# Kernel optimization log

Hardware: AMD Instinct MI355X
Metric: run time of the kernel (lower is better)

## Reference

```python
import jax, jax.numpy as jnp
import numpy as np

N, E, H = 100000, 640000, 64
DIN_N, DIN_E, L, OUT = 32, 16, 2, 1
BN_EPS = 1e-5


def setup_inputs() -> dict:
    key = jax.random.key(0)
    ks = iter(jax.random.split(key, 40))
    def p(shape, s=0.05):
        return jax.random.normal(next(ks), shape, dtype=jnp.float32) * s
    return {
        "x": jax.random.normal(next(ks), (N, DIN_N), dtype=jnp.float32),
        "edge_attr": jax.random.normal(next(ks), (E, DIN_E), dtype=jnp.float32),
        "src": jax.random.randint(next(ks), (E,), 0, N),
        "dst": jax.random.randint(next(ks), (E,), 0, N),
        "node_emb_w": p((DIN_N, H)), "node_emb_b": p((H,)),
        "edge_emb_w": p((DIN_E, H)), "edge_emb_b": p((H,)),
        "lin_edge_w": p((L, H, H)), "lin_edge_b": p((L, H)),
        "conv_w1": p((L, H, H)), "conv_b1": p((L, H)),
        "conv_w2": p((L, H, H)), "conv_b2": p((L, H)),
        "emlp_w1": p((L, 3 * H, H)), "emlp_b1": p((L, H)),
        "emlp_w2": p((L, H, H)), "emlp_b2": p((L, H)),
        "bn_gamma": jnp.ones((L, H), jnp.float32),
        "bn_beta": jnp.zeros((L, H), jnp.float32),
        "mlp_w1": p((3 * H, 50)), "mlp_b1": p((50,)),
        "mlp_w2": p((50, 25)), "mlp_b2": p((25,)),
        "mlp_w3": p((25, OUT)), "mlp_b3": p((OUT,)),
    }


def _batchnorm(h, gamma, beta):
    # training-mode BatchNorm1d over the node axis (biased variance)
    mu = jnp.mean(h, axis=0)
    var = jnp.mean(jnp.square(h - mu), axis=0)
    return gamma * (h - mu) * jax.lax.rsqrt(var + BN_EPS) + beta


def _forward(x, edge_attr, src, dst,
             node_emb_w, node_emb_b, edge_emb_w, edge_emb_b,
             lin_edge_w, lin_edge_b, conv_w1, conv_b1, conv_w2, conv_b2,
             emlp_w1, emlp_b1, emlp_w2, emlp_b2, bn_gamma, bn_beta,
             mlp_w1, mlp_b1, mlp_w2, mlp_b2, mlp_w3, mlp_b3):
    x = x @ node_emb_w + node_emb_b                       # [N, H]
    e = edge_attr @ edge_emb_w + edge_emb_b               # [E, H]
    for i in range(L):
        # GINEConv (eps=0): msg = ReLU(x_src + Lin(edge_attr)); sum at dst
        msg = jax.nn.relu(x[src] + e @ lin_edge_w[i] + lin_edge_b[i])
        agg = jax.ops.segment_sum(msg, dst, num_segments=N)
        h = x + agg
        h = jax.nn.relu(h @ conv_w1[i] + conv_b1[i]) @ conv_w2[i] + conv_b2[i]
        x = (x + jax.nn.relu(_batchnorm(h, bn_gamma[i], bn_beta[i]))) / 2
        cat = jnp.concatenate([x[src], x[dst], e], axis=-1)  # [E, 3H]
        upd = jax.nn.relu(cat @ emlp_w1[i] + emlp_b1[i]) @ emlp_w2[i] + emlp_b2[i]
        e = e + upd / 2
    # edge readout: relu(cat(x_src, x_dst)) ++ edge_attr -> MLP (dropout off/eval)
    er = jnp.concatenate(
        [jax.nn.relu(jnp.concatenate([x[src], x[dst]], axis=-1)), e], axis=-1)
    hmid = jax.nn.relu(er @ mlp_w1 + mlp_b1)
    hmid = jax.nn.relu(hmid @ mlp_w2 + mlp_b2)
    logit = hmid @ mlp_w3 + mlp_b3
    return x, logit


def reference(x, edge_attr, src, dst,
              node_emb_w, node_emb_b, edge_emb_w, edge_emb_b,
              lin_edge_w, lin_edge_b, conv_w1, conv_b1, conv_w2, conv_b2,
              emlp_w1, emlp_b1, emlp_w2, emlp_b2, bn_gamma, bn_beta,
              mlp_w1, mlp_b1, mlp_w2, mlp_b2, mlp_w3, mlp_b3):
    return _forward(x, edge_attr, src, dst,
                    node_emb_w, node_emb_b, edge_emb_w, edge_emb_b,
                    lin_edge_w, lin_edge_b, conv_w1, conv_b1, conv_w2, conv_b2,
                    emlp_w1, emlp_b1, emlp_w2, emlp_b2, bn_gamma, bn_beta,
                    mlp_w1, mlp_b1, mlp_w2, mlp_b2, mlp_w3, mlp_b3)
```

## Files before the change

kernel.cpp:

```cpp
#include <hip/hip_runtime.h>

#define NN 100000
#define NE 640000
#define NB_SCAN 98

typedef __attribute__((ext_vector_type(8))) short short8;
typedef __attribute__((ext_vector_type(4))) float f32x4;
typedef __attribute__((ext_vector_type(4))) ushort ushort4v;

__device__ __forceinline__ float bf2f(ushort u) {
    unsigned v = ((unsigned)u) << 16;
    return __builtin_bit_cast(float, v);
}
__device__ __forceinline__ ushort f2bf(float f) {
    unsigned u = __builtin_bit_cast(unsigned, f);
    u += 0x7fffu + ((u >> 16) & 1u);
    return (ushort)(u >> 16);
}
__device__ __forceinline__ short8 brelu(short8 v) {
    #pragma unroll
    for (int i = 0; i < 8; ++i) v[i] = (v[i] < (short)0) ? (short)0 : v[i];
    return v;
}

__global__ void k_hist(const int* __restrict__ dst, int* __restrict__ hist)
{
    int i = blockIdx.x * 256 + threadIdx.x;
    atomicAdd(&hist[dst[i]], 1);
}

__global__ __launch_bounds__(256) void k_scan_part(const int* __restrict__ hist,
                                                   int* __restrict__ rp,
                                                   int* __restrict__ parts)
{
    __shared__ int s[256];
    int b = blockIdx.x, t = threadIdx.x;
    int base = b * 1024 + t * 4;
    int v[4]; int sum = 0;
    #pragma unroll
    for (int i = 0; i < 4; ++i) { int idx = base + i; v[i] = (idx < NN) ? hist[idx] : 0; sum += v[i]; }
    s[t] = sum; __syncthreads();
    for (int off = 1; off < 256; off <<= 1) {
        int x = (t >= off) ? s[t - off] : 0;
        __syncthreads(); s[t] += x; __syncthreads();
    }
    int excl = s[t] - sum;
    if (t == 255) parts[b] = s[255];
    int run = excl;
    #pragma unroll
    for (int i = 0; i < 4; ++i) { int idx = base + i; if (idx < NN) rp[idx] = run; run += v[i]; }
}

__global__ void k_scan_tops(int* __restrict__ parts, int* __restrict__ rp)
{
    __shared__ int s[128];
    int t = threadIdx.x;
    int v = (t < NB_SCAN) ? parts[t] : 0;
    s[t] = v; __syncthreads();
    for (int off = 1; off < 128; off <<= 1) {
        int x = (t >= off) ? s[t - off] : 0;
        __syncthreads(); s[t] += x; __syncthreads();
    }
    parts[t] = s[t] - v;
    if (t == 0) rp[NN] = NE;
}

__global__ __launch_bounds__(256) void k_scan_add(int* __restrict__ rp,
                                                  const int* __restrict__ parts,
                                                  int* __restrict__ cursor)
{
    int i = blockIdx.x * 256 + threadIdx.x;
    if (i >= NN) return;
    int v = rp[i] + parts[i >> 10];
    rp[i] = v; cursor[i] = v;
}

__global__ void k_scatter(const int* __restrict__ dst,
                          int* __restrict__ cursor, int* __restrict__ eidx)
{
    int i = blockIdx.x * 256 + threadIdx.x;
    int d = dst[i];
    int p = atomicAdd(&cursor[d], 1);
    eidx[p] = i;
}

__global__ void k_w_subtile(const float* __restrict__ w, ushort* __restrict__ out,
                            int K, int Nin)
{
    int t = blockIdx.x * 256 + threadIdx.x;
    if (t >= K * 64) return;
    int k = t >> 6, c = t & 63;
    float v = (c < Nin) ? w[k * Nin + c] : 0.f;
    out[((k >> 3) * 64 + c) * 8 + (k & 7)] = f2bf(v);
}

__global__ void k_w_padk(const float* __restrict__ w, ushort* __restrict__ out,
                         int Kreal, int Kpad)
{
    int t = blockIdx.x * 256 + threadIdx.x;
    if (t >= Kpad * 64) return;
    int k = t >> 6, c = t & 63;
    float v = (k < Kreal) ? w[k * 64 + c] : 0.f;
    out[((k >> 3) * 64 + c) * 8 + (k & 7)] = f2bf(v);
}

__global__ void k_w_msg(const float* __restrict__ lw, ushort* __restrict__ out)
{
    int t = blockIdx.x * 256 + threadIdx.x;
    if (t >= 128 * 64) return;
    int k = t >> 6, c = t & 63;
    float v = (k < 64) ? (k == c ? 1.f : 0.f) : lw[(k - 64) * 64 + c];
    out[((k >> 3) * 64 + c) * 8 + (k & 7)] = f2bf(v);
}

__global__ __launch_bounds__(256) void k_node_emb_mfma(
    const float* __restrict__ xin, const ushort* __restrict__ ws,
    const float* __restrict__ b, float* __restrict__ xout,
    ushort* __restrict__ xb)
{
    __shared__ ushort wl[32 * 64];
    __shared__ float fbuf[4][16 * 64];
    __shared__ ushort bbuf[4][16 * 64];
    int tid = threadIdx.x;
    *(short8*)&wl[tid * 8] = *(const short8*)&ws[tid * 8];
    __syncthreads();

    int wid = tid >> 6, lane = tid & 63, c = lane & 15, kg = lane >> 4;
    int t = blockIdx.x * 4 + wid;
    if (t >= NN / 16) return;
    int n0 = t * 16;

    const float* xr = xin + (size_t)(n0 + c) * 32 + kg * 8;
    f32x4 u0 = *(const f32x4*)xr, u1 = *(const f32x4*)(xr + 4);
    short8 a;
    #pragma unroll
    for (int j = 0; j < 4; ++j) { a[j] = (short)f2bf(u0[j]); a[4 + j] = (short)f2bf(u1[j]); }

    f32x4 acc[4];
    #pragma unroll
    for (int nt = 0; nt < 4; ++nt) {
        float bv = b[nt * 16 + c];
        acc[nt] = f32x4{bv, bv, bv, bv};
        short8 bf = *(const short8*)&wl[(kg * 64 + nt * 16 + c) * 8];
        acc[nt] = __builtin_amdgcn_mfma_f32_16x16x32_bf16(a, bf, acc[nt], 0, 0, 0);
    }
    #pragma unroll
    for (int nt = 0; nt < 4; ++nt)
        #pragma unroll
        for (int i = 0; i < 4; ++i) {
            int rr = kg * 4 + i, cc = nt * 16 + c;
            float v = acc[nt][i];
            fbuf[wid][rr * 64 + cc] = v;
            bbuf[wid][rr * 64 + cc] = f2bf(v);
        }
    #pragma unroll
    for (int r = 0; r < 4; ++r) {
        int q = r * 64 + lane;
        *(f32x4*)&xout[(size_t)(n0 + (q >> 4)) * 64 + (q & 15) * 4] =
            *(f32x4*)&fbuf[wid][q * 4];
    }
    #pragma unroll
    for (int r = 0; r < 2; ++r) {
        int q = r * 64 + lane;
        *(short8*)&xb[(size_t)(n0 + (q >> 3)) * 64 + (q & 7) * 8] =
            *(short8*)&bbuf[wid][q * 8];
    }
}

__global__ __launch_bounds__(256) void k_edge_emb_fused(
    const float* __restrict__ ein, const ushort* __restrict__ ws,
    const float* __restrict__ b, ushort* __restrict__ eb,
    const ushort* __restrict__ xb, const int* __restrict__ src,
    const ushort* __restrict__ wm, const float* __restrict__ lb,
    ushort* __restrict__ msgbuf)
{
    __shared__ ushort wl[32 * 64];
    __shared__ ushort wml[128 * 64];
    __shared__ ushort bbuf[4][16 * 72];
    int tid = threadIdx.x;
    *(short8*)&wl[tid * 8] = *(const short8*)&ws[tid * 8];
    #pragma unroll
    for (int i = 0; i < 4; ++i)
        *(short8*)&wml[(i * 256 + tid) * 8] = *(const short8*)&wm[(i * 256 + tid) * 8];
    __syncthreads();

    int wid = tid >> 6, lane = tid & 63, c = lane & 15, kg = lane >> 4;
    int e0 = (blockIdx.x * 4 + wid) * 16;
    ushort* bb = bbuf[wid];

    const ushort* xs = xb + (size_t)src[e0 + c] * 64;
    short8 a0 = *(const short8*)(xs + kg * 8);
    short8 a1 = *(const short8*)(xs + 32 + kg * 8);

    short8 a = (short8)0;
    if (kg < 2) {
        const float* er = ein + (size_t)(e0 + c) * 16 + kg * 8;
        f32x4 u0 = *(const f32x4*)er, u1 = *(const f32x4*)(er + 4);
        #pragma unroll
        for (int j = 0; j < 4; ++j) { a[j] = (short)f2bf(u0[j]); a[4 + j] = (short)f2bf(u1[j]); }
    }
    f32x4 acc[4];
    #pragma unroll
    for (int nt = 0; nt < 4; ++nt) {
        float bv = b[nt * 16 + c];
        acc[nt] = f32x4{bv, bv, bv, bv};
        short8 bf = *(const short8*)&wl[(kg * 64 + nt * 16 + c) * 8];
        acc[nt] = __builtin_amdgcn_mfma_f32_16x16x32_bf16(a, bf, acc[nt], 0, 0, 0);
    }
    #pragma unroll
    for (int nt = 0; nt < 4; ++nt)
        #pragma unroll
        for (int i = 0; i < 4; ++i)
            bb[(kg * 4 + i) * 72 + nt * 16 + c] = f2bf(acc[nt][i]);
    #pragma unroll
    for (int r = 0; r < 2; ++r) {
        int q = r * 64 + lane;
        *(short8*)&eb[(size_t)(e0 + (q >> 3)) * 64 + (q & 7) * 8] =
            *(short8*)&bb[(q >> 3) * 72 + (q & 7) * 8];
    }
    short8 en0 = *(const short8*)&bb[c * 72 + kg * 8];
    short8 en1 = *(const short8*)&bb[c * 72 + 32 + kg * 8];

    f32x4 acc3[4];
    #pragma unroll
    for (int nt = 0; nt < 4; ++nt) {
        float bv = lb[nt * 16 + c];
        acc3[nt] = f32x4{bv, bv, bv, bv};
    }
    short8 af[4] = {a0, a1, en0, en1};
    #pragma unroll
    for (int ks = 0; ks < 4; ++ks) {
        #pragma unroll
        for (int nt = 0; nt < 4; ++nt) {
            short8 bf = *(const short8*)&wml[((ks * 4 + kg) * 64 + nt * 16 + c) * 8];
            acc3[nt] = __builtin_amdgcn_mfma_f32_16x16x32_bf16(af[ks], bf, acc3[nt], 0, 0, 0);
        }
    }
    #pragma unroll
    for (int nt = 0; nt < 4; ++nt)
        #pragma unroll
        for (int i = 0; i < 4; ++i)
            bb[(kg * 4 + i) * 72 + nt * 16 + c] = f2bf(fmaxf(acc3[nt][i], 0.f));
    #pragma unroll
    for (int r = 0; r < 2; ++r) {
        int q = r * 64 + lane;
        *(short8*)&msgbuf[(size_t)(e0 + (q >> 3)) * 64 + (q & 7) * 8] =
            *(short8*)&bb[(q >> 3) * 72 + (q & 7) * 8];
    }
}

__global__ __launch_bounds__(256) void k_conv_csr(
    const float* __restrict__ x, const ushort* __restrict__ msgbuf,
    const int* __restrict__ rp, const int* __restrict__ eidx,
    float* __restrict__ hout,
    const ushort* __restrict__ w1s, const float* __restrict__ b1,
    const ushort* __restrict__ w2s, const float* __restrict__ b2,
    float* __restrict__ stats)
{
    __shared__ ushort w1l[64 * 64];
    __shared__ ushort w2l[64 * 64];
    __shared__ ushort h1l[4][1024];
    __shared__ float red[2][4][64];
    int tid = threadIdx.x;
    #pragma unroll
    for (int i = 0; i < 2; ++i) {
        *(short8*)&w1l[(i * 256 + tid) * 8] = *(const short8*)&w1s[(i * 256 + tid) * 8];
        *(short8*)&w2l[(i * 256 + tid) * 8] = *(const short8*)&w2s[(i * 256 + tid) * 8];
    }
    __syncthreads();

    int wid = tid >> 6, lane = tid & 63;
    int c = lane & 15, kg = lane >> 4;

    short8 w2f[2][4];
    #pragma unroll
    for (int ks = 0; ks < 2; ++ks)
        #pragma unroll
        for (int nt = 0; nt < 4; ++nt)
            w2f[ks][nt] = *(const short8*)&w2l[((ks * 4 + kg) * 64 + nt * 16 + c) * 8];

    float b1v[4], b2v[4];
    #pragma unroll
    for (int nt = 0; nt < 4; ++nt) { b1v[nt] = b1[nt * 16 + c]; b2v[nt] = b2[nt * 16 + c]; }

    float s1[4] = {0.f, 0.f, 0.f, 0.f}, s2[4] = {0.f, 0.f, 0.f, 0.f};
    ushort* hl = h1l[wid];

    int t = blockIdx.x * 4 + wid;
    if (t < NN / 16) {
        int n0 = t * 16;
        int n = n0 + c;
        int jb = rp[n], je = rp[n + 1];
        float sm0[8] = {0,0,0,0,0,0,0,0}, sm1[8] = {0,0,0,0,0,0,0,0};
        if (jb < je) {
            int row = eidx[jb];
            short8 m0 = *(const short8*)&msgbuf[(size_t)row * 64 + kg * 8];
            short8 m1 = *(const short8*)&msgbuf[(size_t)row * 64 + 32 + kg * 8];
            for (int j = jb + 1; j <= je; ++j) {
                short8 p0, p1;
                if (j < je) {
                    int nrow = eidx[j];
                    p0 = *(const short8*)&msgbuf[(size_t)nrow * 64 + kg * 8];
                    p1 = *(const short8*)&msgbuf[(size_t)nrow * 64 + 32 + kg * 8];
                }
                #pragma unroll
                for (int i = 0; i < 8; ++i) {
                    sm0[i] += bf2f((ushort)m0[i]);
                    sm1[i] += bf2f((ushort)m1[i]);
                }
                if (j < je) { m0 = p0; m1 = p1; }
            }
        }
        const float* xr = x + (size_t)n * 64;
        f32x4 u0 = *(const f32x4*)(xr + kg * 8);
        f32x4 u1 = *(const f32x4*)(xr + kg * 8 + 4);
        f32x4 v0 = *(const f32x4*)(xr + 32 + kg * 8);
        f32x4 v1 = *(const f32x4*)(xr + 32 + kg * 8 + 4);
        short8 a[2];
        #pragma unroll
        for (int j = 0; j < 4; ++j) {
            a[0][j]     = (short)f2bf(u0[j] + sm0[j]);
            a[0][4 + j] = (short)f2bf(u1[j] + sm0[4 + j]);
            a[1][j]     = (short)f2bf(v0[j] + sm1[j]);
            a[1][4 + j] = (short)f2bf(v1[j] + sm1[4 + j]);
        }
        f32x4 acc[4];
        #pragma unroll
        for (int nt = 0; nt < 4; ++nt) acc[nt] = f32x4{b1v[nt], b1v[nt], b1v[nt], b1v[nt]};
        #pragma unroll
        for (int ks = 0; ks < 2; ++ks) {
            #pragma unroll
            for (int nt = 0; nt < 4; ++nt) {
                short8 bf = *(const short8*)&w1l[((ks * 4 + kg) * 64 + nt * 16 + c) * 8];
                acc[nt] = __builtin_amdgcn_mfma_f32_16x16x32_bf16(a[ks], bf, acc[nt], 0, 0, 0);
            }
        }
        #pragma unroll
        for (int nt = 0; nt < 4; ++nt) {
            #pragma unroll
            for (int i = 0; i < 4; ++i) {
                int rr = kg * 4 + i, cc = nt * 16 + c;
                hl[((cc >> 3) * 16 + rr) * 8 + (cc & 7)] = f2bf(fmaxf(acc[nt][i], 0.f));
            }
        }
        f32x4 acc2[4];
        #pragma unroll
        for (int nt = 0; nt < 4; ++nt) acc2[nt] = f32x4{b2v[nt], b2v[nt], b2v[nt], b2v[nt]};
        #pragma unroll
        for (int ks = 0; ks < 2; ++ks) {
            short8 ha = *(const short8*)&hl[((ks * 4 + kg) * 16 + c) * 8];
            #pragma unroll
            for (int nt = 0; nt < 4; ++nt)
                acc2[nt] = __builtin_amdgcn_mfma_f32_16x16x32_bf16(ha, w2f[ks][nt], acc2[nt], 0, 0, 0);
        }
        #pragma unroll
        for (int nt = 0; nt < 4; ++nt) {
            #pragma unroll
            for (int i = 0; i < 4; ++i) {
                int rr = kg * 4 + i, cc = nt * 16 + c;
                float h2 = acc2[nt][i];
                hout[(size_t)(n0 + rr) * 64 + cc] = h2;
                s1[nt] += h2;
                s2[nt] += h2 * h2;
            }
        }
    }
    #pragma unroll
    for (int nt = 0; nt < 4; ++nt) {
        float v1 = s1[nt], v2 = s2[nt];
        v1 += __shfl_xor(v1, 16); v1 += __shfl_xor(v1, 32);
        v2 += __shfl_xor(v2, 16); v2 += __shfl_xor(v2, 32);
        s1[nt] = v1; s2[nt] = v2;
    }
    if (lane < 16) {
        #pragma unroll
        for (int nt = 0; nt < 4; ++nt) {
            red[0][wid][nt * 16 + c] = s1[nt];
            red[1][wid][nt * 16 + c] = s2[nt];
        }
    }
    __syncthreads();
    if (wid == 0) {
        float a = red[0][0][lane] + red[0][1][lane] + red[0][2][lane] + red[0][3][lane];
        float b = red[1][0][lane] + red[1][1][lane] + red[1][2][lane] + red[1][3][lane];
        unsafeAtomicAdd(&stats[lane], a);
        unsafeAtomicAdd(&stats[64 + lane], b);
    }
}

__global__ void k_bnfin(float* __restrict__ stats,
                        const float* __restrict__ gamma,
                        const float* __restrict__ beta)
{
    int j = threadIdx.x;
    float mu = stats[j] * (1.f / NN);
    float var = stats[64 + j] * (1.f / NN) - mu * mu;
    float a = gamma[j] * rsqrtf(var + 1e-5f);
    stats[128 + j] = a;
    stats[192 + j] = beta[j] - mu * a;
}

__global__ __launch_bounds__(256) void k_xupd4(float* __restrict__ x,
                                               const float* __restrict__ h,
                                               const float* __restrict__ stats,
                                               ushort* __restrict__ xb)
{
    int idx = blockIdx.x * 256 + threadIdx.x;
    int j4 = (idx & 15) * 4;
    f32x4 hv = *(const f32x4*)&h[(size_t)idx * 4];
    f32x4 xv = *(const f32x4*)&x[(size_t)idx * 4];
    f32x4 av = *(const f32x4*)&stats[128 + j4];
    f32x4 cv = *(const f32x4*)&stats[192 + j4];
    f32x4 xo;
    ushort4v bo;
    #pragma unroll
    for (int i = 0; i < 4; ++i) {
        float r = fmaxf(fmaf(hv[i], av[i], cv[i]), 0.f);
        float xn = (xv[i] + r) * 0.5f;
        xo[i] = xn;
        bo[i] = f2bf(xn);
    }
    *(f32x4*)&x[(size_t)idx * 4] = xo;
    *(ushort4v*)&xb[(size_t)idx * 4] = bo;
}

template<int NEXT>
__global__ __launch_bounds__(256) void k_emlp_fused(
    const ushort* __restrict__ xb, ushort* __restrict__ eb,
    const int* __restrict__ src, const int* __restrict__ dst,
    const ushort* __restrict__ w1s, const float* __restrict__ b1,
    const ushort* __restrict__ w2s, const float* __restrict__ b2,
    const ushort* __restrict__ wm, const float* __restrict__ lbn,
    ushort* __restrict__ msgbuf)
{
    __shared__ ushort w1l[192 * 64];
    __shared__ ushort wml[NEXT ? 128 * 64 : 8];
    __shared__ ushort hb[4][1152];
    int tid = threadIdx.x;
    #pragma unroll
    for (int i = 0; i < 6; ++i)
        *(short8*)&w1l[(i * 256 + tid) * 8] = *(const short8*)&w1s[(i * 256 + tid) * 8];
    if (NEXT) {
        #pragma unroll
        for (int i = 0; i < 4; ++i)
            *(short8*)&wml[(i * 256 + tid) * 8] = *(const short8*)&wm[(i * 256 + tid) * 8];
    }
    __syncthreads();

    int wid = tid >> 6, lane = tid & 63;
    int c = lane & 15, kg = lane >> 4;

    short8 w2f[2][4];
    #pragma unroll
    for (int ks = 0; ks < 2; ++ks)
        #pragma unroll
        for (int nt = 0; nt < 4; ++nt)
            w2f[ks][nt] = *(const short8*)&w2s[((ks * 4 + kg) * 64 + nt * 16 + c) * 8];

    float b1v[4], b2v[4], lbv[4];
    #pragma unroll
    for (int nt = 0; nt < 4; ++nt) {
        b1v[nt] = b1[nt * 16 + c];
        b2v[nt] = b2[nt * 16 + c];
        lbv[nt] = NEXT ? lbn[nt * 16 + c] : 0.f;
    }
    ushort* hl = hb[wid];

    int ebase = blockIdx.x * 256 + wid * 64;

    short8 a[6];
    {
        int myedge = ebase + c;
        int s = src[myedge], d = dst[myedge];
        const ushort* xs = xb + (size_t)s * 64;
        const ushort* xd = xb + (size_t)d * 64;
        const ushort* ee = eb + (size_t)myedge * 64;
        a[0] = *(const short8*)(xs + kg * 8);
        a[1] = *(const short8*)(xs + 32 + kg * 8);
        a[2] = *(const short8*)(xd + kg * 8);
        a[3] = *(const short8*)(xd + 32 + kg * 8);
        a[4] = *(const short8*)(ee + kg * 8);
        a[5] = *(const short8*)(ee + 32 + kg * 8);
    }

    #pragma unroll 1
    for (int t4 = 0; t4 < 4; ++t4) {
        int e0 = ebase + t4 * 16;
        int myedge = e0 + c;

        short8 an[6];
        if (t4 < 3) {
            int sn = src[myedge + 16];
            int dn = dst[myedge + 16];
            const ushort* xsn = xb + (size_t)sn * 64;
            const ushort* xdn = xb + (size_t)dn * 64;
            const ushort* een = eb + (size_t)(myedge + 16) * 64;
            an[0] = *(const short8*)(xsn + kg * 8);
            an[1] = *(const short8*)(xsn + 32 + kg * 8);
            an[2] = *(const short8*)(xdn + kg * 8);
            an[3] = *(const short8*)(xdn + 32 + kg * 8);
            an[4] = *(const short8*)(een + kg * 8);
            an[5] = *(const short8*)(een + 32 + kg * 8);
        }

        f32x4 acc[4];
        #pragma unroll
        for (int nt = 0; nt < 4; ++nt) acc[nt] = f32x4{b1v[nt], b1v[nt], b1v[nt], b1v[nt]};
        #pragma unroll
        for (int ks = 0; ks < 6; ++ks) {
            #pragma unroll
            for (int nt = 0; nt < 4; ++nt) {
                short8 bf = *(const short8*)&w1l[((ks * 4 + kg) * 64 + nt * 16 + c) * 8];
                acc[nt] = __builtin_amdgcn_mfma_f32_16x16x32_bf16(a[ks], bf, acc[nt], 0, 0, 0);
            }
        }
        #pragma unroll
        for (int nt = 0; nt < 4; ++nt) {
            #pragma unroll
            for (int i = 0; i < 4; ++i) {
                int rr = kg * 4 + i, cc = nt * 16 + c;
                hl[((cc >> 3) * 16 + rr) * 8 + (cc & 7)] = f2bf(fmaxf(acc[nt][i], 0.f));
            }
        }
        f32x4 acc2[4];
        #pragma unroll
        for (int nt = 0; nt < 4; ++nt) acc2[nt] = f32x4{b2v[nt], b2v[nt], b2v[nt], b2v[nt]};
        #pragma unroll
        for (int ks = 0; ks < 2; ++ks) {
            short8 ha = *(const short8*)&hl[((ks * 4 + kg) * 16 + c) * 8];
            #pragma unroll
            for (int nt = 0; nt < 4; ++nt)
                acc2[nt] = __builtin_amdgcn_mfma_f32_16x16x32_bf16(ha, w2f[ks][nt], acc2[nt], 0, 0, 0);
        }
        #pragma unroll
        for (int nt = 0; nt < 4; ++nt)
            #pragma unroll
            for (int i = 0; i < 4; ++i)
                hl[(kg * 4 + i) * 72 + nt * 16 + c] = f2bf(acc2[nt][i]);
        short8 u0 = *(const short8*)&hl[c * 72 + kg * 8];
        short8 u1 = *(const short8*)&hl[c * 72 + 32 + kg * 8];
        short8 en0, en1;
        #pragma unroll
        for (int j = 0; j < 8; ++j) {
            en0[j] = (short)f2bf(bf2f((ushort)a[4][j]) + 0.5f * bf2f((ushort)u0[j]));
            en1[j] = (short)f2bf(bf2f((ushort)a[5][j]) + 0.5f * bf2f((ushort)u1[j]));
        }
        *(short8*)&eb[(size_t)myedge * 64 + kg * 8]      = en0;
        *(short8*)&eb[(size_t)myedge * 64 + 32 + kg * 8] = en1;

        if (NEXT) {
            f32x4 acc3[4];
            #pragma unroll
            for (int nt = 0; nt < 4; ++nt) acc3[nt] = f32x4{lbv[nt], lbv[nt], lbv[nt], lbv[nt]};
            short8 af[4] = {a[0], a[1], en0, en1};
            #pragma unroll
            for (int ks = 0; ks < 4; ++ks) {
                #pragma unroll
                for (int nt = 0; nt < 4; ++nt) {
                    short8 bf = *(const short8*)&wml[((ks * 4 + kg) * 64 + nt * 16 + c) * 8];
                    acc3[nt] = __builtin_amdgcn_mfma_f32_16x16x32_bf16(af[ks], bf, acc3[nt], 0, 0, 0);
                }
            }
            #pragma unroll
            for (int nt = 0; nt < 4; ++nt)
                #pragma unroll
                for (int i = 0; i < 4; ++i)
                    hl[(kg * 4 + i) * 72 + nt * 16 + c] = f2bf(fmaxf(acc3[nt][i], 0.f));
            #pragma unroll
            for (int r = 0; r < 2; ++r) {
                int q = r * 64 + lane;
                *(short8*)&msgbuf[(size_t)(e0 + (q >> 3)) * 64 + (q & 7) * 8] =
                    *(short8*)&hl[(q >> 3) * 72 + (q & 7) * 8];
            }
        }

        if (t4 < 3) {
            #pragma unroll
            for (int i = 0; i < 6; ++i) a[i] = an[i];
        }
    }
}

__global__ __launch_bounds__(256) void k_readout_mfma(
    const ushort* __restrict__ xb, const ushort* __restrict__ eb,
    const int* __restrict__ src, const int* __restrict__ dst,
    const ushort* __restrict__ w1s, const float* __restrict__ b1,
    const float* __restrict__ w2, const float* __restrict__ b2,
    const float* __restrict__ w3, const float* __restrict__ b3,
    float* __restrict__ logit)
{
    __shared__ ushort w1l[192 * 64];
    __shared__ ushort hw[4][64 * 50];
    int tid = threadIdx.x;
    #pragma unroll
    for (int i = 0; i < 6; ++i)
        *(short8*)&w1l[(i * 256 + tid) * 8] = *(const short8*)&w1s[(i * 256 + tid) * 8];
    __syncthreads();

    int wid = tid >> 6, lane = tid & 63;
    int c = lane & 15, kg = lane >> 4;
    float b1v[4];
    #pragma unroll
    for (int nt = 0; nt < 4; ++nt) b1v[nt] = (nt * 16 + c < 50) ? b1[nt * 16 + c] : 0.f;

    int ebase = blockIdx.x * 256 + wid * 64;

    short8 a[6];
    {
        int myedge = ebase + c;
        int s = src[myedge], d = dst[myedge];
        const ushort* xs = xb + (size_t)s * 64;
        const ushort* xd = xb + (size_t)d * 64;
        const ushort* ee = eb + (size_t)myedge * 64;
        a[0] = *(const short8*)(xs + kg * 8);
        a[1] = *(const short8*)(xs + 32 + kg * 8);
        a[2] = *(const short8*)(xd + kg * 8);
        a[3] = *(const short8*)(xd + 32 + kg * 8);
        a[4] = *(const short8*)(ee + kg * 8);
        a[5] = *(const short8*)(ee + 32 + kg * 8);
    }

    #pragma unroll 1
    for (int t4 = 0; t4 < 4; ++t4) {
        int e0 = ebase + t4 * 16;
        int myedge = e0 + c;

        short8 an[6];
        if (t4 < 3) {
            int sn = src[myedge + 16];
            int dn = dst[myedge + 16];
            const ushort* xsn = xb + (size_t)sn * 64;
            const ushort* xdn = xb + (size_t)dn * 64;
            const ushort* een = eb + (size_t)(myedge + 16) * 64;
            an[0] = *(const short8*)(xsn + kg * 8);
            an[1] = *(const short8*)(xsn + 32 + kg * 8);
            an[2] = *(const short8*)(xdn + kg * 8);
            an[3] = *(const short8*)(xdn + 32 + kg * 8);
            an[4] = *(const short8*)(een + kg * 8);
            an[5] = *(const short8*)(een + 32 + kg * 8);
        }

        short8 af[6];
        af[0] = brelu(a[0]); af[1] = brelu(a[1]);
        af[2] = brelu(a[2]); af[3] = brelu(a[3]);
        af[4] = a[4];        af[5] = a[5];

        f32x4 acc[4];
        #pragma unroll
        for (int nt = 0; nt < 4; ++nt) acc[nt] = f32x4{b1v[nt], b1v[nt], b1v[nt], b1v[nt]};
        #pragma unroll
        for (int ks = 0; ks < 6; ++ks) {
            #pragma unroll
            for (int nt = 0; nt < 4; ++nt) {
                short8 bf = *(const short8*)&w1l[((ks * 4 + kg) * 64 + nt * 16 + c) * 8];
                acc[nt] = __builtin_amdgcn_mfma_f32_16x16x32_bf16(af[ks], bf, acc[nt], 0, 0, 0);
            }
        }
        #pragma unroll
        for (int nt = 0; nt < 4; ++nt) {
            #pragma unroll
            for (int i = 0; i < 4; ++i) {
                int rr = kg * 4 + i, cc = nt * 16 + c;
                if (cc < 50)
                    hw[wid][(t4 * 16 + rr) * 50 + cc] = f2bf(fmaxf(acc[nt][i], 0.f));
            }
        }
        if (t4 < 3) {
            #pragma unroll
            for (int i = 0; i < 6; ++i) a[i] = an[i];
        }
    }
    int edge = blockIdx.x * 256 + wid * 64 + lane;
    const ushort* hrow = &hw[wid][lane * 50];
    float a25[25];
    #pragma unroll
    for (int j = 0; j < 25; ++j) a25[j] = b2[j];
    #pragma unroll 2
    for (int k = 0; k < 50; ++k) {
        float hv = bf2f(hrow[k]);
        #pragma unroll
        for (int j = 0; j < 25; ++j) a25[j] = fmaf(hv, w2[k * 25 + j], a25[j]);
    }
    float lg = b3[0];
    #pragma unroll
    for (int k = 0; k < 25; ++k) lg = fmaf(fmaxf(a25[k], 0.f), w3[k], lg);
    logit[edge] = lg;
}

extern "C" void kernel_launch(void* const* d_in, const int* in_sizes, int n_in,
                              void* d_out, int out_size, void* d_ws, size_t ws_size,
                              hipStream_t stream)
{
    const float* x_in  = (const float*)d_in[0];
    const float* eattr = (const float*)d_in[1];
    const int*   src   = (const int*)d_in[2];
    const int*   dst   = (const int*)d_in[3];
    const float* n_w   = (const float*)d_in[4];
    const float* n_b   = (const float*)d_in[5];
    const float* e_w   = (const float*)d_in[6];
    const float* e_b   = (const float*)d_in[7];
    const float* lw    = (const float*)d_in[8];
    const float* lb    = (const float*)d_in[9];
    const float* cw1   = (const float*)d_in[10];
    const float* cb1   = (const float*)d_in[11];
    const float* cw2   = (const float*)d_in[12];
    const float* cb2   = (const float*)d_in[13];
    const float* ew1   = (const float*)d_in[14];
    const float* eb1   = (const float*)d_in[15];
    const float* ew2   = (const float*)d_in[16];
    const float* eb2   = (const float*)d_in[17];
    const float* gam   = (const float*)d_in[18];
    const float* bet   = (const float*)d_in[19];
    const float* m1w   = (const float*)d_in[20];
    const float* m1b   = (const float*)d_in[21];
    const float* m2w   = (const float*)d_in[22];
    const float* m2b   = (const float*)d_in[23];
    const float* m3w   = (const float*)d_in[24];
    const float* m3b   = (const float*)d_in[25];

    float* xbuf  = (float*)d_out;
    float* logit = xbuf + (size_t)NN * 64;

    ushort* eb     = (ushort*)d_ws;
    float*  tmp    = (float*)(eb + (size_t)NE * 64);
    float*  stats  = tmp + (size_t)NN * 64;
    ushort* w1s    = (ushort*)(stats + 512);
    ushort* w2s    = w1s + 2 * 192 * 64;
    ushort* m1s    = w2s + 2 * 64 * 64;
    ushort* xb     = m1s + 192 * 64;
    ushort* wms    = xb + (size_t)NN * 64;
    ushort* cw1s   = wms + 2 * 128 * 64;
    ushort* cw2s   = cw1s + 2 * 64 * 64;
    ushort* nws    = cw2s + 2 * 64 * 64;
    ushort* ews    = nws + 32 * 64;
    ushort* msgbuf = ews + 32 * 64;
    int*    hist   = (int*)(msgbuf + (size_t)NE * 64);
    int*    rp     = hist + NN;
    int*    cursor = rp + NN + 1;
    int*    parts  = cursor + NN;
    int*    eidx   = parts + 128;

    hipMemsetAsync(hist, 0, NN * sizeof(int), stream);
    hipMemsetAsync(stats, 0, 512 * sizeof(float), stream);
    k_hist<<<NE / 256, 256, 0, stream>>>(dst, hist);
    k_scan_part<<<NB_SCAN, 256, 0, stream>>>(hist, rp, parts);
    k_scan_tops<<<1, 128, 0, stream>>>(parts, rp);
    k_scan_add<<<(NN + 255) / 256, 256, 0, stream>>>(rp, parts, cursor);
    k_scatter<<<NE / 256, 256, 0, stream>>>(dst, cursor, eidx);

    k_w_subtile<<<48, 256, 0, stream>>>(ew1,            w1s,            192, 64);
    k_w_subtile<<<48, 256, 0, stream>>>(ew1 + 192 * 64, w1s + 192 * 64, 192, 64);
    k_w_subtile<<<16, 256, 0, stream>>>(ew2,            w2s,            64, 64);
    k_w_subtile<<<16, 256, 0, stream>>>(ew2 + 64 * 64,  w2s + 64 * 64,  64, 64);
    k_w_subtile<<<48, 256, 0, stream>>>(m1w,            m1s,            192, 50);
    k_w_msg<<<32, 256, 0, stream>>>(lw,           wms);
    k_w_msg<<<32, 256, 0, stream>>>(lw + 64 * 64, wms + 128 * 64);
    k_w_subtile<<<16, 256, 0, stream>>>(cw1,            cw1s,           64, 64);
    k_w_subtile<<<16, 256, 0, stream>>>(cw1 + 64 * 64,  cw1s + 64 * 64, 64, 64);
    k_w_subtile<<<16, 256, 0, stream>>>(cw2,            cw2s,           64, 64);
    k_w_subtile<<<16, 256, 0, stream>>>(cw2 + 64 * 64,  cw2s + 64 * 64, 64, 64);
    k_w_padk<<<8, 256, 0, stream>>>(n_w, nws, 32, 32);
    k_w_padk<<<8, 256, 0, stream>>>(e_w, ews, 16, 32);

    k_node_emb_mfma<<<(NN / 16 + 3) / 4, 256, 0, stream>>>(x_in, nws, n_b, xbuf, xb);
    k_edge_emb_fused<<<NE / 64, 256, 0, stream>>>(eattr, ews, e_b, eb,
                                                  xb, src, wms, lb, msgbuf);

    for (int l = 0; l < 2; ++l) {
        float* st = stats + l * 256;
        k_conv_csr<<<(NN / 16 + 3) / 4, 256, 0, stream>>>(
            xbuf, msgbuf, rp, eidx, tmp, cw1s + l * 64 * 64, cb1 + l * 64,
            cw2s + l * 64 * 64, cb2 + l * 64, st);
        k_bnfin<<<1, 64, 0, stream>>>(st, gam + l * 64, bet + l * 64);
        k_xupd4<<<NN * 16 / 256, 256, 0, stream>>>(xbuf, tmp, st, xb);
        if (l == 0) {
            k_emlp_fused<1><<<NE / 256, 256, 0, stream>>>(
                xb, eb, src, dst, w1s, eb1, w2s, eb2,
                wms + 128 * 64, lb + 64, msgbuf);
        } else {
            k_emlp_fused<0><<<NE / 256, 256, 0, stream>>>(
                xb, eb, src, dst, w1s + 192 * 64, eb1 + 64, w2s + 64 * 64, eb2 + 64,
                wms, lb, msgbuf);
        }
    }

    k_readout_mfma<<<NE / 256, 256, 0, stream>>>(xb, eb, src, dst,
                                                 m1s, m1b, m2w, m2b, m3w, m3b, logit);
}
```

Measured before the change: 537.4 us.

## Process two 16-edge tiles per iteration in edge MLP kernel, move W2 to LDS

The fused edge-MLP kernel now handles two 16-edge tiles (A and B) per loop iteration, interleaving their MFMA chains so independent work can hide MFMA latency. It prefetches the next pair of tiles' gathers after the first GEMM. The second-layer weights move from per-thread register fragments into shared memory to free registers for the doubled accumulators and operands. LDS use grows (double h buffer plus W2), and register pressure rises, which may lower occupancy.

Result: slower. 562.6 us (+4.7%).

```diff
diff --git a/kernel.cpp b/kernel.cpp
--- a/kernel.cpp
+++ b/kernel.cpp
@@ -434,12 +434,16 @@
     ushort* __restrict__ msgbuf)
 {
     __shared__ ushort w1l[192 * 64];
+    __shared__ ushort w2l[64 * 64];
     __shared__ ushort wml[NEXT ? 128 * 64 : 8];
-    __shared__ ushort hb[4][1152];
+    __shared__ ushort hb[4][2304];
     int tid = threadIdx.x;
     #pragma unroll
     for (int i = 0; i < 6; ++i)
         *(short8*)&w1l[(i * 256 + tid) * 8] = *(const short8*)&w1s[(i * 256 + tid) * 8];
+    #pragma unroll
+    for (int i = 0; i < 2; ++i)
+        *(short8*)&w2l[(i * 256 + tid) * 8] = *(const short8*)&w2s[(i * 256 + tid) * 8];
     if (NEXT) {
         #pragma unroll
         for (int i = 0; i < 4; ++i)
@@ -449,13 +453,6 @@
 
     int wid = tid >> 6, lane = tid & 63;
     int c = lane & 15, kg = lane >> 4;
-
-    short8 w2f[2][4];
-    #pragma unroll
-    for (int ks = 0; ks < 2; ++ks)
-        #pragma unroll
-        for (int nt = 0; nt < 4; ++nt)
-            w2f[ks][nt] = *(const short8*)&w2s[((ks * 4 + kg) * 64 + nt * 16 + c) * 8];
 
     float b1v[4], b2v[4], lbv[4];
     #pragma unroll
@@ -464,119 +461,176 @@
         b2v[nt] = b2[nt * 16 + c];
         lbv[nt] = NEXT ? lbn[nt * 16 + c] : 0.f;
     }
-    ushort* hl = hb[wid];
+    ushort* hlA = hb[wid];
+    ushort* hlB = hb[wid] + 1152;
 
     int ebase = blockIdx.x * 256 + wid * 64;
 
-    short8 a[6];
+    short8 aA[6], aB[6];
     {
-        int myedge = ebase + c;
-        int s = src[myedge], d = dst[myedge];
-        const ushort* xs = xb + (size_t)s * 64;
-        const ushort* xd = xb + (size_t)d * 64;
-        const ushort* ee = eb + (size_t)myedge * 64;
-        a[0] = *(const short8*)(xs + kg * 8);
-        a[1] = *(const short8*)(xs + 32 + kg * 8);
-        a[2] = *(const short8*)(xd + kg * 8);
-        a[3] = *(const short8*)(xd + 32 + kg * 8);
-        a[4] = *(const short8*)(ee + kg * 8);
-        a[5] = *(const short8*)(ee + 32 + kg * 8);
+        int mA = ebase + c, mB = ebase + 16 + c;
+        int sA = src[mA], dA = dst[mA];
+        int sB = src[mB], dB = dst[mB];
+        const ushort* xsA = xb + (size_t)sA * 64;
+        const ushort* xdA = xb + (size_t)dA * 64;
+        const ushort* eeA = eb + (size_t)mA * 64;
+        const ushort* xsB = xb + (size_t)sB * 64;
+        const ushort* xdB = xb + (size_t)dB * 64;
+        const ushort* eeB = eb + (size_t)mB * 64;
+        aA[0] = *(const short8*)(xsA + kg * 8);
+        aA[1] = *(const short8*)(xsA + 32 + kg * 8);
+        aA[2] = *(const short8*)(xdA + kg * 8);
+        aA[3] = *(const short8*)(xdA + 32 + kg * 8);
+        aA[4] = *(const short8*)(eeA + kg * 8);
+        aA[5] = *(const short8*)(eeA + 32 + kg * 8);
+        aB[0] = *(const short8*)(xsB + kg * 8);
+        aB[1] = *(const short8*)(xsB + 32 + kg * 8);
+        aB[2] = *(const short8*)(xdB + kg * 8);
+        aB[3] = *(const short8*)(xdB + 32 + kg * 8);
+        aB[4] = *(const short8*)(eeB + kg * 8);
+        aB[5] = *(const short8*)(eeB + 32 + kg * 8);
     }
 
     #pragma unroll 1
-    for (int t4 = 0; t4 < 4; ++t4) {
-        int e0 = ebase + t4 * 16;
-        int myedge = e0 + c;
-
-        short8 an[6];
-        if (t4 < 3) {
-            int sn = src[myedge + 16];
-            int dn = dst[myedge + 16];
-            const ushort* xsn = xb + (size_t)sn * 64;
-            const ushort* xdn = xb + (size_t)dn * 64;
-            const ushort* een = eb + (size_t)(myedge + 16) * 64;
-            an[0] = *(const short8*)(xsn + kg * 8);
-            an[1] = *(const short8*)(xsn + 32 + kg * 8);
-            an[2] = *(const short8*)(xdn + kg * 8);
-            an[3] = *(const short8*)(xdn + 32 + kg * 8);
-            an[4] = *(const short8*)(een + kg * 8);
-            an[5] = *(const short8*)(een + 32 + kg * 8);
-        }
-
-        f32x4 acc[4];
-        #pragma unroll
-        for (int nt = 0; nt < 4; ++nt) acc[nt] = f32x4{b1v[nt], b1v[nt], b1v[nt], b1v[nt]};
+    for (int pr = 0; pr < 2; ++pr) {
+        int e0A = ebase + pr * 32;
+        int e0B = e0A + 16;
+        int mA = e0A + c, mB = e0B + c;
+
+        f32x4 accA[4], accB[4];
+        #pragma unroll
+        for (int nt = 0; nt < 4; ++nt) {
+            accA[nt] = f32x4{b1v[nt], b1v[nt], b1v[nt], b1v[nt]};
+            accB[nt] = f32x4{b1v[nt], b1v[nt], b1v[nt], b1v[nt]};
+        }
         #pragma unroll
         for (int ks = 0; ks < 6; ++ks) {
             #pragma unroll
             for (int nt = 0; nt < 4; ++nt) {
                 short8 bf = *(const short8*)&w1l[((ks * 4 + kg) * 64 + nt * 16 + c) * 8];
-                acc[nt] = __builtin_amdgcn_mfma_f32_16x16x32_bf16(a[ks], bf, acc[nt], 0, 0, 0);
-            }
-        }
+                accA[nt] = __builtin_amdgcn_mfma_f32_16x16x32_bf16(aA[ks], bf, accA[nt], 0, 0, 0);
+                accB[nt] = __builtin_amdgcn_mfma_f32_16x16x32_bf16(aB[ks], bf, accB[nt], 0, 0, 0);
+            }
+        }
+
+        short8 nA[6], nB[6];
+        if (pr == 0) {
+            int pA = mA + 32, pB = mB + 32;
+            int sA = src[pA], dA = dst[pA];
+            int sB = src[pB], dB = dst[pB];
+            const ushort* xsA = xb + (size_t)sA * 64;
+            const ushort* xdA = xb + (size_t)dA * 64;
+            const ushort* eeA = eb + (size_t)pA * 64;
+            const ushort* xsB = xb + (size_t)sB * 64;
+            const ushort* xdB = xb + (size_t)dB * 64;
+            const ushort* eeB = eb + (size_t)pB * 64;
+            nA[0] = *(const short8*)(xsA + kg * 8);
+            nA[1] = *(const short8*)(xsA + 32 + kg * 8);
+            nA[2] = *(const short8*)(xdA + kg * 8);
+            nA[3] = *(const short8*)(xdA + 32 + kg * 8);
+            nA[4] = *(const short8*)(eeA + kg * 8);
+            nA[5] = *(const short8*)(eeA + 32 + kg * 8);
+            nB[0] = *(const short8*)(xsB + kg * 8);
+            nB[1] = *(const short8*)(xsB + 32 + kg * 8);
+            nB[2] = *(const short8*)(xdB + kg * 8);
+            nB[3] = *(const short8*)(xdB + 32 + kg * 8);
+            nB[4] = *(const short8*)(eeB + kg * 8);
+            nB[5] = *(const short8*)(eeB + 32 + kg * 8);
+        }
+
         #pragma unroll
         for (int nt = 0; nt < 4; ++nt) {
             #pragma unroll
             for (int i = 0; i < 4; ++i) {
                 int rr = kg * 4 + i, cc = nt * 16 + c;
-                hl[((cc >> 3) * 16 + rr) * 8 + (cc & 7)] = f2bf(fmaxf(acc[nt][i], 0.f));
-            }
-        }
-        f32x4 acc2[4];
-        #pragma unroll
-        for (int nt = 0; nt < 4; ++nt) acc2[nt] = f32x4{b2v[nt], b2v[nt], b2v[nt], b2v[nt]};
+                int off = ((cc >> 3) * 16 + rr) * 8 + (cc & 7);
+                hlA[off] = f2bf(fmaxf(accA[nt][i], 0.f));
+                hlB[off] = f2bf(fmaxf(accB[nt][i], 0.f));
+            }
+        }
+        f32x4 a2A[4], a2B[4];
+        #pragma unroll
+        for (int nt = 0; nt < 4; ++nt) {
+            a2A[nt] = f32x4{b2v[nt], b2v[nt], b2v[nt], b2v[nt]};
+            a2B[nt] = f32x4{b2v[nt], b2v[nt], b2v[nt], b2v[nt]};
+        }
         #pragma unroll
         for (int ks = 0; ks < 2; ++ks) {
-            short8 ha = *(const short8*)&hl[((ks * 4 + kg) * 16 + c) * 8];
-            #pragma unroll
-            for (int nt = 0; nt < 4; ++nt)
-                acc2[nt] = __builtin_amdgcn_mfma_f32_16x16x32_bf16(ha, w2f[ks][nt], acc2[nt], 0, 0, 0);
-        }
-        #pragma unroll
-        for (int nt = 0; nt < 4; ++nt)
-            #pragma unroll
-            for (int i = 0; i < 4; ++i)
-                hl[(kg * 4 + i) * 72 + nt * 16 + c] = f2bf(acc2[nt][i]);
-        short8 u0 = *(const short8*)&hl[c * 72 + kg * 8];
-        short8 u1 = *(const short8*)&hl[c * 72 + 32 + kg * 8];
-        short8 en0, en1;
+            short8 haA = *(const short8*)&hlA[((ks * 4 + kg) * 16 + c) * 8];
+            short8 haB = *(const short8*)&hlB[((ks * 4 + kg) * 16 + c) * 8];
+            #pragma unroll
+            for (int nt = 0; nt < 4; ++nt) {
+                short8 bw = *(const short8*)&w2l[((ks * 4 + kg) * 64 + nt * 16 + c) * 8];
+                a2A[nt] = __builtin_amdgcn_mfma_f32_16x16x32_bf16(haA, bw, a2A[nt], 0, 0, 0);
+                a2B[nt] = __builtin_amdgcn_mfma_f32_16x16x32_bf16(haB, bw, a2B[nt], 0, 0, 0);
+            }
+        }
+        #pragma unroll
+        for (int nt = 0; nt < 4; ++nt) {
+            #pragma unroll
+            for (int i = 0; i < 4; ++i) {
+                int off = (kg * 4 + i) * 72 + nt * 16 + c;
+                hlA[off] = f2bf(a2A[nt][i]);
+                hlB[off] = f2bf(a2B[nt][i]);
+            }
+        }
+        short8 u0A = *(const short8*)&hlA[c * 72 + kg * 8];
+        short8 u1A = *(const short8*)&hlA[c * 72 + 32 + kg * 8];
+        short8 u0B = *(const short8*)&hlB[c * 72 + kg * 8];
+        short8 u1B = *(const short8*)&hlB[c * 72 + 32 + kg * 8];
+        short8 enA0, enA1, enB0, enB1;
         #pragma unroll
         for (int j = 0; j < 8; ++j) {
-            en0[j] = (short)f2bf(bf2f((ushort)a[4][j]) + 0.5f * bf2f((ushort)u0[j]));
-            en1[j] = (short)f2bf(bf2f((ushort)a[5][j]) + 0.5f * bf2f((ushort)u1[j]));
-        }
-        *(short8*)&eb[(size_t)myedge * 64 + kg * 8]      = en0;
-        *(short8*)&eb[(size_t)myedge * 64 + 32 + kg * 8] = en1;
+            enA0[j] = (short)f2bf(bf2f((ushort)aA[4][j]) + 0.5f * bf2f((ushort)u0A[j]));
+            enA1[j] = (short)f2bf(bf2f((ushort)aA[5][j]) + 0.5f * bf2f((ushort)u1A[j]));
+            enB0[j] = (short)f2bf(bf2f((ushort)aB[4][j]) + 0.5f * bf2f((ushort)u0B[j]));
+            enB1[j] = (short)f2bf(bf2f((ushort)aB[5][j]) + 0.5f * bf2f((ushort)u1B[j]));
+        }
+        *(short8*)&eb[(size_t)mA * 64 + kg * 8]      = enA0;
+        *(short8*)&eb[(size_t)mA * 64 + 32 + kg * 8] = enA1;
+        *(short8*)&eb[(size_t)mB * 64 + kg * 8]      = enB0;
+        *(short8*)&eb[(size_t)mB * 64 + 32 + kg * 8] = enB1;
 
         if (NEXT) {
-            f32x4 acc3[4];
-            #pragma unroll
-            for (int nt = 0; nt < 4; ++nt) acc3[nt] = f32x4{lbv[nt], lbv[nt], lbv[nt], lbv[nt]};
-            short8 af[4] = {a[0], a[1], en0, en1};
+            f32x4 a3A[4], a3B[4];
+            #pragma unroll
+            for (int nt = 0; nt < 4; ++nt) {
+                a3A[nt] = f32x4{lbv[nt], lbv[nt], lbv[nt], lbv[nt]};
+                a3B[nt] = f32x4{lbv[nt], lbv[nt], lbv[nt], lbv[nt]};
+            }
+            short8 afA[4] = {aA[0], aA[1], enA0, enA1};
+            short8 afB[4] = {aB[0], aB[1], enB0, enB1};
             #pragma unroll
             for (int ks = 0; ks < 4; ++ks) {
                 #pragma unroll
                 for (int nt = 0; nt < 4; ++nt) {
                     short8 bf = *(const short8*)&wml[((ks * 4 + kg) * 64 + nt * 16 + c) * 8];
-                    acc3[nt] = __builtin_amdgcn_mfma_f32_16x16x32_bf16(af[ks], bf, acc3[nt], 0, 0, 0);
+                    a3A[nt] = __builtin_amdgcn_mfma_f32_16x16x32_bf16(afA[ks], bf, a3A[nt], 0, 0, 0);
+                    a3B[nt] = __builtin_amdgcn_mfma_f32_16x16x32_bf16(afB[ks], bf, a3B[nt], 0, 0, 0);
                 }
             }
             #pragma unroll
-            for (int nt = 0; nt < 4; ++nt)
+            for (int nt = 0; nt < 4; ++nt) {
                 #pragma unroll
-                for (int i = 0; i < 4; ++i)
-                    hl[(kg * 4 + i) * 72 + nt * 16 + c] = f2bf(fmaxf(acc3[nt][i], 0.f));
+                for (int i = 0; i < 4; ++i) {
+                    int off = (kg * 4 + i) * 72 + nt * 16 + c;
+                    hlA[off] = f2bf(fmaxf(a3A[nt][i], 0.f));
+                    hlB[off] = f2bf(fmaxf(a3B[nt][i], 0.f));
+                }
+            }
             #pragma unroll
             for (int r = 0; r < 2; ++r) {
                 int q = r * 64 + lane;
-                *(short8*)&msgbuf[(size_t)(e0 + (q >> 3)) * 64 + (q & 7) * 8] =
-                    *(short8*)&hl[(q >> 3) * 72 + (q & 7) * 8];
-            }
-        }
-
-        if (t4 < 3) {
-            #pragma unroll
-            for (int i = 0; i < 6; ++i) a[i] = an[i];
+                *(short8*)&msgbuf[(size_t)(e0A + (q >> 3)) * 64 + (q & 7) * 8] =
+                    *(short8*)&hlA[(q >> 3) * 72 + (q & 7) * 8];
+                *(short8*)&msgbuf[(size_t)(e0B + (q >> 3)) * 64 + (q & 7) * 8] =
+                    *(short8*)&hlB[(q >> 3) * 72 + (q & 7) * 8];
+            }
+        }
+
+        if (pr == 0) {
+            #pragma unroll
+            for (int i = 0; i < 6; ++i) { aA[i] = nA[i]; aB[i] = nB[i]; }
         }
     }
 }
```
